# Kernel tuning notes

Measured on AMD Instinct MI355X. Metric: run time of the kernel, lower is better.

The kernel has to match this reference:

```python
import jax, jax.numpy as jnp
import numpy as np
import math

B, S, D, H, DFF = 4, 1024, 1024, 16, 4096
DK = D // H
EPS = 1e-5


def setup_inputs() -> dict:
    key = jax.random.key(0)
    ks = jax.random.split(key, 16)
    sc = 0.02
    inp = {
        "x": jax.random.normal(ks[0], (B, S, D), jnp.float32),
        "Wq": jax.random.normal(ks[1], (D, D), jnp.float32) * sc,
        "bq": jnp.zeros((D,), jnp.float32),
        "Wk": jax.random.normal(ks[2], (D, D), jnp.float32) * sc,
        "bk": jnp.zeros((D,), jnp.float32),
        "Wv": jax.random.normal(ks[3], (D, D), jnp.float32) * sc,
        "bv": jnp.zeros((D,), jnp.float32),
        "Wo": jax.random.normal(ks[4], (D, D), jnp.float32) * sc,
        "bo": jnp.zeros((D,), jnp.float32),
        "W1": jax.random.normal(ks[5], (D, DFF), jnp.float32) * sc,
        "b1": jnp.zeros((DFF,), jnp.float32),
        "W2": jax.random.normal(ks[6], (DFF, D), jnp.float32) * sc,
        "b2": jnp.zeros((D,), jnp.float32),
        "g1": jnp.ones((D,), jnp.float32),
        "be1": jnp.zeros((D,), jnp.float32),
        "g2": jnp.ones((D,), jnp.float32),
        "be2": jnp.zeros((D,), jnp.float32),
    }
    return inp


def _layernorm(x, g, b):
    mu = jnp.mean(x, axis=-1, keepdims=True)
    var = jnp.mean(jnp.square(x - mu), axis=-1, keepdims=True)
    return (x - mu) * jax.lax.rsqrt(var + EPS) * g + b


def reference(x, Wq, bq, Wk, bk, Wv, bv, Wo, bo, W1, b1, W2, b2, g1, be1, g2, be2):
    # multi-head self-attention (dropout = identity, eval mode)
    q = (x @ Wq + bq).reshape(B, S, H, DK).transpose(0, 2, 1, 3)  # [B,H,S,DK]
    k = (x @ Wk + bk).reshape(B, S, H, DK).transpose(0, 2, 1, 3)
    v = (x @ Wv + bv).reshape(B, S, H, DK).transpose(0, 2, 1, 3)
    scores = jnp.einsum("bhqd,bhkd->bhqk", q, k) / math.sqrt(DK)
    attn_weights = jax.nn.softmax(scores, axis=-1)
    ctx = jnp.einsum("bhqk,bhkd->bhqd", attn_weights, v)
    ctx = ctx.transpose(0, 2, 1, 3).reshape(B, S, D)
    attn_out = ctx @ Wo + bo
    x = _layernorm(x + attn_out, g1, be1)
    ff = jax.nn.relu(x @ W1 + b1) @ W2 + b2
    x = _layernorm(x + ff, g2, be2)
    return x, attn_weights
```

## Files before the change

### kernel.cpp

```cpp
#include <hip/hip_runtime.h>

typedef unsigned short u16;
typedef __attribute__((ext_vector_type(8))) short bf16x8;
typedef __attribute__((ext_vector_type(8))) unsigned short u16x8;
typedef __attribute__((ext_vector_type(4))) float f32x4;

__device__ __forceinline__ u16 f2b(float f) {
  unsigned u = __float_as_uint(f);
  u += 0x7fffu + ((u >> 16) & 1u);
  return (u16)(u >> 16);
}

__global__ __launch_bounds__(256) void cast_k(const float* __restrict__ s,
                                              u16* __restrict__ d, int n4) {
  int i = blockIdx.x * 256 + threadIdx.x;
  if (i >= n4) return;
  float4 v = *(const float4*)(s + (size_t)i * 4);
  ushort4 o = make_ushort4(f2b(v.x), f2b(v.y), f2b(v.z), f2b(v.w));
  *(ushort4*)(d + (size_t)i * 4) = o;
}

__global__ __launch_bounds__(256) void transpose_k(const float* __restrict__ src,
                                                   u16* __restrict__ dst,
                                                   int ldsrc, int lddst) {
  __shared__ float t[32][33];
  int c0 = blockIdx.x * 32, r0 = blockIdx.y * 32;
  int tx = threadIdx.x, ty = threadIdx.y;
#pragma unroll
  for (int i = 0; i < 4; ++i)
    t[ty + i * 8][tx] = src[(size_t)(r0 + ty + i * 8) * ldsrc + c0 + tx];
  __syncthreads();
#pragma unroll
  for (int i = 0; i < 4; ++i)
    dst[(size_t)(c0 + ty + i * 8) * lddst + r0 + tx] = f2b(t[tx][ty + i * 8]);
}

__global__ __launch_bounds__(256) void transpose_v_k(const u16* __restrict__ qkv,
                                                     u16* __restrict__ vt) {
  __shared__ u16 t[32][33];
  int z = blockIdx.z;
  int b = z >> 4, h = z & 15;
  int s0 = blockIdx.x * 32, d0 = blockIdx.y * 32;
  int tx = threadIdx.x, ty = threadIdx.y;
  const u16* src = qkv + (size_t)(b * 1024) * 3072 + 2048 + h * 64;
  u16* dst = vt + (size_t)z * 65536;
#pragma unroll
  for (int i = 0; i < 4; ++i)
    t[ty + i * 8][tx] = src[(size_t)(s0 + ty + i * 8) * 3072 + d0 + tx];
  __syncthreads();
#pragma unroll
  for (int i = 0; i < 4; ++i)
    dst[(size_t)(d0 + ty + i * 8) * 1024 + s0 + tx] = t[tx][ty + i * 8];
}

template <int BN, int AF32, int BIAS, int RELU, int SB16, int SF32>
__global__ __launch_bounds__(256) void gemm_k(
    const u16* __restrict__ Ab, const float* __restrict__ Af,
    long aHi, long aLo, int lda,
    const u16* __restrict__ Bt, long bHi, long bLo, int ldb,
    float* __restrict__ Cf, u16* __restrict__ Cb,
    long cHi, long cLo, int ldc,
    const float* __restrict__ bias, int K, int ZD) {
  constexpr int NT = BN / 32;
  __shared__ u16 As[128 * 40];
  __shared__ u16 Bs[BN * 40];

  const int tid = threadIdx.x;
  const int lane = tid & 63;
  const int wave = tid >> 6;
  const int waveM = wave >> 1, waveN = wave & 1;
  const int quad = lane >> 4, l16 = lane & 15;

  const int zb = blockIdx.z / ZD, zr = blockIdx.z % ZD;
  const long aOff = zb * aHi + zr * aLo;
  const long bOff = zb * bHi + zr * bLo;
  const long cOff = zb * cHi + zr * cLo;

  const int row0 = blockIdx.y * 128;
  const int col0 = blockIdx.x * BN;

  f32x4 acc[4][NT] = {};

  for (int k0 = 0; k0 < K; k0 += 32) {
#pragma unroll
    for (int it = 0; it < 2; ++it) {
      int e = (it * 256 + tid) * 8;
      int r = e >> 5, c = e & 31;
      if (AF32) {
        const float4* p = (const float4*)(Af + aOff + (long)(row0 + r) * lda + k0 + c);
        float4 v0 = p[0], v1 = p[1];
        u16x8 wv;
        wv[0] = f2b(v0.x); wv[1] = f2b(v0.y); wv[2] = f2b(v0.z); wv[3] = f2b(v0.w);
        wv[4] = f2b(v1.x); wv[5] = f2b(v1.y); wv[6] = f2b(v1.z); wv[7] = f2b(v1.w);
        *(u16x8*)&As[r * 40 + c] = wv;
      } else {
        uint4 v = *(const uint4*)(Ab + aOff + (long)(row0 + r) * lda + k0 + c);
        *(uint4*)&As[r * 40 + c] = v;
      }
    }
#pragma unroll
    for (int it = 0; it < BN / 64; ++it) {
      int e = (it * 256 + tid) * 8;
      int r = e >> 5, c = e & 31;
      uint4 v = *(const uint4*)(Bt + bOff + (long)(col0 + r) * ldb + k0 + c);
      *(uint4*)&Bs[r * 40 + c] = v;
    }
    __syncthreads();

    bf16x8 af[4], bfr[NT];
#pragma unroll
    for (int mi = 0; mi < 4; ++mi)
      af[mi] = *(const bf16x8*)&As[(waveM * 64 + mi * 16 + l16) * 40 + quad * 8];
#pragma unroll
    for (int ni = 0; ni < NT; ++ni)
      bfr[ni] = *(const bf16x8*)&Bs[(waveN * (BN / 2) + ni * 16 + l16) * 40 + quad * 8];
#pragma unroll
    for (int mi = 0; mi < 4; ++mi)
#pragma unroll
      for (int ni = 0; ni < NT; ++ni)
        acc[mi][ni] = __builtin_amdgcn_mfma_f32_16x16x32_bf16(af[mi], bfr[ni], acc[mi][ni], 0, 0, 0);
    __syncthreads();
  }

#pragma unroll
  for (int ni = 0; ni < NT; ++ni) {
    int col = col0 + waveN * (BN / 2) + ni * 16 + l16;
    float bv = BIAS ? bias[col] : 0.f;
#pragma unroll
    for (int mi = 0; mi < 4; ++mi) {
#pragma unroll
      for (int r = 0; r < 4; ++r) {
        int row = row0 + waveM * 64 + mi * 16 + quad * 4 + r;
        float v = acc[mi][ni][r] + bv;
        if (RELU) v = fmaxf(v, 0.f);
        long idx = cOff + (long)row * ldc + col;
        if (SF32) Cf[idx] = v;
        if (SB16) Cb[idx] = f2b(v);
      }
    }
  }
}

__global__ __launch_bounds__(256) void softmax_k(float* __restrict__ a) {
  long row = blockIdx.x;
  int tid = threadIdx.x;
  float* p = a + row * 1024 + tid * 4;
  float4 v = *(const float4*)p;
  float m = fmaxf(fmaxf(v.x, v.y), fmaxf(v.z, v.w));
#pragma unroll
  for (int d = 32; d > 0; d >>= 1) m = fmaxf(m, __shfl_xor(m, d));
  __shared__ float red[4];
  if ((tid & 63) == 0) red[tid >> 6] = m;
  __syncthreads();
  m = fmaxf(fmaxf(red[0], red[1]), fmaxf(red[2], red[3]));
  v.x = __expf((v.x - m) * 0.125f);
  v.y = __expf((v.y - m) * 0.125f);
  v.z = __expf((v.z - m) * 0.125f);
  v.w = __expf((v.w - m) * 0.125f);
  float s = v.x + v.y + v.z + v.w;
#pragma unroll
  for (int d = 32; d > 0; d >>= 1) s += __shfl_xor(s, d);
  __shared__ float red2[4];
  if ((tid & 63) == 0) red2[tid >> 6] = s;
  __syncthreads();
  s = red2[0] + red2[1] + red2[2] + red2[3];
  float r = 1.f / s;
  v.x *= r; v.y *= r; v.z *= r; v.w *= r;
  *(float4*)p = v;
}

template <int WB16>
__global__ __launch_bounds__(256) void add_ln_k(const float* __restrict__ xp,
                                                const float* __restrict__ yp,
                                                const float* __restrict__ g,
                                                const float* __restrict__ bta,
                                                float* __restrict__ of,
                                                u16* __restrict__ ob) {
  long row = blockIdx.x;
  int tid = threadIdx.x;
  const float4 xv = *(const float4*)(xp + row * 1024 + tid * 4);
  const float4 yv = *(const float4*)(yp + row * 1024 + tid * 4);
  float4 v = make_float4(xv.x + yv.x, xv.y + yv.y, xv.z + yv.z, xv.w + yv.w);
  float s1 = v.x + v.y + v.z + v.w;
  float s2 = v.x * v.x + v.y * v.y + v.z * v.z + v.w * v.w;
#pragma unroll
  for (int d = 32; d > 0; d >>= 1) {
    s1 += __shfl_xor(s1, d);
    s2 += __shfl_xor(s2, d);
  }
  __shared__ float r1[4], r2[4];
  if ((tid & 63) == 0) { r1[tid >> 6] = s1; r2[tid >> 6] = s2; }
  __syncthreads();
  s1 = r1[0] + r1[1] + r1[2] + r1[3];
  s2 = r2[0] + r2[1] + r2[2] + r2[3];
  float mu = s1 * (1.f / 1024.f);
  float var = s2 * (1.f / 1024.f) - mu * mu;
  float rs = rsqrtf(var + 1e-5f);
  float4 gv = *(const float4*)(g + tid * 4);
  float4 bv = *(const float4*)(bta + tid * 4);
  float4 o;
  o.x = (v.x - mu) * rs * gv.x + bv.x;
  o.y = (v.y - mu) * rs * gv.y + bv.y;
  o.z = (v.z - mu) * rs * gv.z + bv.z;
  o.w = (v.w - mu) * rs * gv.w + bv.w;
  *(float4*)(of + row * 1024 + tid * 4) = o;
  if (WB16) {
    ushort4 ov = make_ushort4(f2b(o.x), f2b(o.y), f2b(o.z), f2b(o.w));
    *(ushort4*)(ob + row * 1024 + tid * 4) = ov;
  }
}

extern "C" void kernel_launch(void* const* d_in, const int* in_sizes, int n_in,
                              void* d_out, int out_size, void* d_ws, size_t ws_size,
                              hipStream_t stream) {
  const float* x   = (const float*)d_in[0];
  const float* Wq  = (const float*)d_in[1];
  const float* bq  = (const float*)d_in[2];
  const float* Wk  = (const float*)d_in[3];
  const float* bk  = (const float*)d_in[4];
  const float* Wv  = (const float*)d_in[5];
  const float* bv  = (const float*)d_in[6];
  const float* Wo  = (const float*)d_in[7];
  const float* bo  = (const float*)d_in[8];
  const float* W1  = (const float*)d_in[9];
  const float* b1  = (const float*)d_in[10];
  const float* W2  = (const float*)d_in[11];
  const float* b2  = (const float*)d_in[12];
  const float* g1  = (const float*)d_in[13];
  const float* be1 = (const float*)d_in[14];
  const float* g2  = (const float*)d_in[15];
  const float* be2 = (const float*)d_in[16];

  float* out = (float*)d_out;
  float* attn = out + 4194304LL;

  char* w = (char*)d_ws;
  size_t off = 0;
  auto alloc = [&](size_t bytes) {
    void* p = w + off;
    off = (off + bytes + 255) & ~(size_t)255;
    return p;
  };
  u16* xb        = (u16*)alloc(8388608);
  u16* Wqkvt     = (u16*)alloc(6291456);
  u16* Wot       = (u16*)alloc(2097152);
  u16* W1t       = (u16*)alloc(8388608);
  u16* W2t       = (u16*)alloc(8388608);
  float* bqkv    = (float*)alloc(12288);
  u16* qkvb      = (u16*)alloc(25165824);
  u16* vtb       = (u16*)alloc(8388608);
  u16* ctxb      = (u16*)alloc(8388608);
  float* attn_o  = (float*)alloc(16777216);
  float* x1      = (float*)alloc(16777216);
  u16* x1b       = (u16*)alloc(8388608);
  u16* ff1b      = (u16*)alloc(33554432);
  float* ff2     = (float*)alloc(16777216);
  (void)ws_size; (void)in_sizes; (void)n_in; (void)out_size;

  dim3 tb(32, 8);
  cast_k<<<4096, 256, 0, stream>>>(x, xb, 1048576);
  transpose_k<<<dim3(32, 32), tb, 0, stream>>>(Wq, Wqkvt,           1024, 1024);
  transpose_k<<<dim3(32, 32), tb, 0, stream>>>(Wk, Wqkvt + 1048576, 1024, 1024);
  transpose_k<<<dim3(32, 32), tb, 0, stream>>>(Wv, Wqkvt + 2097152, 1024, 1024);
  transpose_k<<<dim3(32, 32), tb, 0, stream>>>(Wo, Wot, 1024, 1024);
  transpose_k<<<dim3(128, 32), tb, 0, stream>>>(W1, W1t, 4096, 1024);
  transpose_k<<<dim3(32, 128), tb, 0, stream>>>(W2, W2t, 1024, 4096);
  hipMemcpyAsync(bqkv,        bq, 4096, hipMemcpyDeviceToDevice, stream);
  hipMemcpyAsync(bqkv + 1024, bk, 4096, hipMemcpyDeviceToDevice, stream);
  hipMemcpyAsync(bqkv + 2048, bv, 4096, hipMemcpyDeviceToDevice, stream);

  gemm_k<128, 0, 1, 0, 1, 0><<<dim3(24, 32, 1), 256, 0, stream>>>(
      xb, nullptr, 0, 0, 1024, Wqkvt, 0, 0, 1024,
      nullptr, qkvb, 0, 0, 3072, bqkv, 1024, 1);

  transpose_v_k<<<dim3(32, 2, 64), tb, 0, stream>>>(qkvb, vtb);

  gemm_k<128, 0, 0, 0, 0, 1><<<dim3(8, 8, 64), 256, 0, stream>>>(
      qkvb, nullptr, 3145728, 64, 3072,
      qkvb + 1024, 3145728, 64, 3072,
      attn, nullptr, 16777216, 1048576, 1024, nullptr, 64, 16);

  softmax_k<<<65536, 256, 0, stream>>>(attn);

  gemm_k<64, 1, 0, 0, 1, 0><<<dim3(1, 8, 64), 256, 0, stream>>>(
      nullptr, attn, 16777216, 1048576, 1024,
      vtb, 1048576, 65536, 1024,
      nullptr, ctxb, 1048576, 64, 1024, nullptr, 1024, 16);

  gemm_k<128, 0, 1, 0, 0, 1><<<dim3(8, 32, 1), 256, 0, stream>>>(
      ctxb, nullptr, 0, 0, 1024, Wot, 0, 0, 1024,
      attn_o, nullptr, 0, 0, 1024, bo, 1024, 1);

  add_ln_k<1><<<4096, 256, 0, stream>>>(x, attn_o, g1, be1, x1, x1b);

  gemm_k<128, 0, 1, 1, 1, 0><<<dim3(32, 32, 1), 256, 0, stream>>>(
      x1b, nullptr, 0, 0, 1024, W1t, 0, 0, 1024,
      nullptr, ff1b, 0, 0, 4096, b1, 1024, 1);

  gemm_k<128, 0, 1, 0, 0, 1><<<dim3(8, 32, 1), 256, 0, stream>>>(
      ff1b, nullptr, 0, 0, 4096, W2t, 0, 0, 4096,
      ff2, nullptr, 0, 0, 1024, b2, 4096, 1);

  add_ln_k<0><<<4096, 256, 0, stream>>>(x1, ff2, g2, be2, out, nullptr);
}
```

Before: 822.7 us.

## Use direct global-to-LDS loads in GEMM and restructure softmax via fused exp

The GEMM kernel now stages tiles with global_load_lds 16-byte loads into unpadded LDS, and its K-step goes from 32 to 64 with two MFMA sub-steps per tile. Softmax is split up: the QK^T GEMM applies exp(score/8) in its epilogue and writes bf16, a light norm kernel computes row sums and writes the normalized fp32 weights plus the inverse sums, and the PV GEMM reads the bf16 exponentials and scales each row by the inverse sum. This drops the fp32 read-modify-write pass over the 256MB attention matrix and the fp32-to-bf16 conversion in the PV A-loads. In exchange, the max subtraction is gone, which risks overflow for large scores, and the unpadded LDS layout may cause bank conflicts.

```diff
diff --git a/kernel.cpp b/kernel.cpp
--- a/kernel.cpp
+++ b/kernel.cpp
@@ -2,13 +2,20 @@
 
 typedef unsigned short u16;
 typedef __attribute__((ext_vector_type(8))) short bf16x8;
-typedef __attribute__((ext_vector_type(8))) unsigned short u16x8;
 typedef __attribute__((ext_vector_type(4))) float f32x4;
 
 __device__ __forceinline__ u16 f2b(float f) {
   unsigned u = __float_as_uint(f);
   u += 0x7fffu + ((u >> 16) & 1u);
   return (u16)(u >> 16);
+}
+__device__ __forceinline__ float b2f(u16 v) {
+  return __uint_as_float((unsigned)v << 16);
+}
+
+__device__ __forceinline__ void gload16(const u16* g, u16* l) {
+  __builtin_amdgcn_global_load_lds((__attribute__((address_space(1))) void*)(g),
+                                   (__attribute__((address_space(3))) void*)(l), 16, 0, 0);
 }
 
 __global__ __launch_bounds__(256) void cast_k(const float* __restrict__ s,
@@ -53,17 +60,18 @@
     dst[(size_t)(d0 + ty + i * 8) * 1024 + s0 + tx] = t[tx][ty + i * 8];
 }
 
-template <int BN, int AF32, int BIAS, int RELU, int SB16, int SF32>
+template <int BN, int BIAS, int RELU, int EXPE, int RSCALE, int SB16, int SF32>
 __global__ __launch_bounds__(256) void gemm_k(
-    const u16* __restrict__ Ab, const float* __restrict__ Af,
-    long aHi, long aLo, int lda,
+    const u16* __restrict__ Ab, long aHi, long aLo, int lda,
     const u16* __restrict__ Bt, long bHi, long bLo, int ldb,
     float* __restrict__ Cf, u16* __restrict__ Cb,
     long cHi, long cLo, int ldc,
-    const float* __restrict__ bias, int K, int ZD) {
+    const float* __restrict__ bias, const float* __restrict__ rs,
+    int K, int ZD) {
   constexpr int NT = BN / 32;
-  __shared__ u16 As[128 * 40];
-  __shared__ u16 Bs[BN * 40];
+  constexpr int CB = (BN * 64 * 2) / 1024;
+  __shared__ __align__(128) u16 As[128 * 64];
+  __shared__ __align__(128) u16 Bs[BN * 64];
 
   const int tid = threadIdx.x;
   const int lane = tid & 63;
@@ -79,46 +87,44 @@
   const int row0 = blockIdx.y * 128;
   const int col0 = blockIdx.x * BN;
 
+  const int lr = lane >> 3;
+  const int lc = (lane & 7) * 8;
+
   f32x4 acc[4][NT] = {};
 
-  for (int k0 = 0; k0 < K; k0 += 32) {
-#pragma unroll
-    for (int it = 0; it < 2; ++it) {
-      int e = (it * 256 + tid) * 8;
-      int r = e >> 5, c = e & 31;
-      if (AF32) {
-        const float4* p = (const float4*)(Af + aOff + (long)(row0 + r) * lda + k0 + c);
-        float4 v0 = p[0], v1 = p[1];
-        u16x8 wv;
-        wv[0] = f2b(v0.x); wv[1] = f2b(v0.y); wv[2] = f2b(v0.z); wv[3] = f2b(v0.w);
-        wv[4] = f2b(v1.x); wv[5] = f2b(v1.y); wv[6] = f2b(v1.z); wv[7] = f2b(v1.w);
-        *(u16x8*)&As[r * 40 + c] = wv;
-      } else {
-        uint4 v = *(const uint4*)(Ab + aOff + (long)(row0 + r) * lda + k0 + c);
-        *(uint4*)&As[r * 40 + c] = v;
-      }
+  for (int k0 = 0; k0 < K; k0 += 64) {
+    const u16* Ag = Ab + aOff + (long)row0 * lda + k0;
+    const u16* Bg = Bt + bOff + (long)col0 * ldb + k0;
+#pragma unroll
+    for (int c = 0; c < 4; ++c) {
+      int ch = c * 4 + wave;
+      gload16(Ag + (long)(ch * 8 + lr) * lda + lc, &As[ch * 512]);
     }
 #pragma unroll
-    for (int it = 0; it < BN / 64; ++it) {
-      int e = (it * 256 + tid) * 8;
-      int r = e >> 5, c = e & 31;
-      uint4 v = *(const uint4*)(Bt + bOff + (long)(col0 + r) * ldb + k0 + c);
-      *(uint4*)&Bs[r * 40 + c] = v;
+    for (int c = 0; c < CB / 4; ++c) {
+      int ch = c * 4 + wave;
+      gload16(Bg + (long)(ch * 8 + lr) * ldb + lc, &Bs[ch * 512]);
     }
     __syncthreads();
 
-    bf16x8 af[4], bfr[NT];
+    bf16x8 af[4][2], bfr[NT][2];
 #pragma unroll
     for (int mi = 0; mi < 4; ++mi)
-      af[mi] = *(const bf16x8*)&As[(waveM * 64 + mi * 16 + l16) * 40 + quad * 8];
+#pragma unroll
+      for (int ks = 0; ks < 2; ++ks)
+        af[mi][ks] = *(const bf16x8*)&As[(waveM * 64 + mi * 16 + l16) * 64 + ks * 32 + quad * 8];
 #pragma unroll
     for (int ni = 0; ni < NT; ++ni)
-      bfr[ni] = *(const bf16x8*)&Bs[(waveN * (BN / 2) + ni * 16 + l16) * 40 + quad * 8];
-#pragma unroll
-    for (int mi = 0; mi < 4; ++mi)
-#pragma unroll
-      for (int ni = 0; ni < NT; ++ni)
-        acc[mi][ni] = __builtin_amdgcn_mfma_f32_16x16x32_bf16(af[mi], bfr[ni], acc[mi][ni], 0, 0, 0);
+#pragma unroll
+      for (int ks = 0; ks < 2; ++ks)
+        bfr[ni][ks] = *(const bf16x8*)&Bs[(waveN * (BN / 2) + ni * 16 + l16) * 64 + ks * 32 + quad * 8];
+#pragma unroll
+    for (int ks = 0; ks < 2; ++ks)
+#pragma unroll
+      for (int mi = 0; mi < 4; ++mi)
+#pragma unroll
+        for (int ni = 0; ni < NT; ++ni)
+          acc[mi][ni] = __builtin_amdgcn_mfma_f32_16x16x32_bf16(af[mi][ks], bfr[ni][ks], acc[mi][ni], 0, 0, 0);
     __syncthreads();
   }
 
@@ -133,6 +139,8 @@
         int row = row0 + waveM * 64 + mi * 16 + quad * 4 + r;
         float v = acc[mi][ni][r] + bv;
         if (RELU) v = fmaxf(v, 0.f);
+        if (EXPE) v = __expf(v * 0.125f);
+        if (RSCALE) v *= rs[(long)blockIdx.z * 1024 + row];
         long idx = cOff + (long)row * ldc + col;
         if (SF32) Cf[idx] = v;
         if (SB16) Cb[idx] = f2b(v);
@@ -141,32 +149,25 @@
   }
 }
 
-__global__ __launch_bounds__(256) void softmax_k(float* __restrict__ a) {
+__global__ __launch_bounds__(256) void norm_k(const u16* __restrict__ e,
+                                              float* __restrict__ w,
+                                              float* __restrict__ inv) {
   long row = blockIdx.x;
   int tid = threadIdx.x;
-  float* p = a + row * 1024 + tid * 4;
-  float4 v = *(const float4*)p;
-  float m = fmaxf(fmaxf(v.x, v.y), fmaxf(v.z, v.w));
-#pragma unroll
-  for (int d = 32; d > 0; d >>= 1) m = fmaxf(m, __shfl_xor(m, d));
+  ushort4 ev = *(const ushort4*)(e + row * 1024 + tid * 4);
+  float4 v;
+  v.x = b2f(ev.x); v.y = b2f(ev.y); v.z = b2f(ev.z); v.w = b2f(ev.w);
+  float s = v.x + v.y + v.z + v.w;
+#pragma unroll
+  for (int d = 32; d > 0; d >>= 1) s += __shfl_xor(s, d);
   __shared__ float red[4];
-  if ((tid & 63) == 0) red[tid >> 6] = m;
+  if ((tid & 63) == 0) red[tid >> 6] = s;
   __syncthreads();
-  m = fmaxf(fmaxf(red[0], red[1]), fmaxf(red[2], red[3]));
-  v.x = __expf((v.x - m) * 0.125f);
-  v.y = __expf((v.y - m) * 0.125f);
-  v.z = __expf((v.z - m) * 0.125f);
-  v.w = __expf((v.w - m) * 0.125f);
-  float s = v.x + v.y + v.z + v.w;
-#pragma unroll
-  for (int d = 32; d > 0; d >>= 1) s += __shfl_xor(s, d);
-  __shared__ float red2[4];
-  if ((tid & 63) == 0) red2[tid >> 6] = s;
-  __syncthreads();
-  s = red2[0] + red2[1] + red2[2] + red2[3];
+  s = red[0] + red[1] + red[2] + red[3];
   float r = 1.f / s;
-  v.x *= r; v.y *= r; v.z *= r; v.w *= r;
-  *(float4*)p = v;
+  float4 o = make_float4(v.x * r, v.y * r, v.z * r, v.w * r);
+  *(float4*)(w + row * 1024 + tid * 4) = o;
+  if (tid == 0) inv[row] = r;
 }
 
 template <int WB16>
@@ -249,6 +250,8 @@
   float* bqkv    = (float*)alloc(12288);
   u16* qkvb      = (u16*)alloc(25165824);
   u16* vtb       = (u16*)alloc(8388608);
+  u16* expb      = (u16*)alloc(134217728);
+  float* inv     = (float*)alloc(262144);
   u16* ctxb      = (u16*)alloc(8388608);
   float* attn_o  = (float*)alloc(16777216);
   float* x1      = (float*)alloc(16777216);
@@ -269,37 +272,37 @@
   hipMemcpyAsync(bqkv + 1024, bk, 4096, hipMemcpyDeviceToDevice, stream);
   hipMemcpyAsync(bqkv + 2048, bv, 4096, hipMemcpyDeviceToDevice, stream);
 
-  gemm_k<128, 0, 1, 0, 1, 0><<<dim3(24, 32, 1), 256, 0, stream>>>(
-      xb, nullptr, 0, 0, 1024, Wqkvt, 0, 0, 1024,
-      nullptr, qkvb, 0, 0, 3072, bqkv, 1024, 1);
+  gemm_k<128, 1, 0, 0, 0, 1, 0><<<dim3(24, 32, 1), 256, 0, stream>>>(
+      xb, 0, 0, 1024, Wqkvt, 0, 0, 1024,
+      nullptr, qkvb, 0, 0, 3072, bqkv, nullptr, 1024, 1);
 
   transpose_v_k<<<dim3(32, 2, 64), tb, 0, stream>>>(qkvb, vtb);
 
-  gemm_k<128, 0, 0, 0, 0, 1><<<dim3(8, 8, 64), 256, 0, stream>>>(
-      qkvb, nullptr, 3145728, 64, 3072,
-      qkvb + 1024, 3145728, 64, 3072,
-      attn, nullptr, 16777216, 1048576, 1024, nullptr, 64, 16);
-
-  softmax_k<<<65536, 256, 0, stream>>>(attn);
-
-  gemm_k<64, 1, 0, 0, 1, 0><<<dim3(1, 8, 64), 256, 0, stream>>>(
-      nullptr, attn, 16777216, 1048576, 1024,
-      vtb, 1048576, 65536, 1024,
-      nullptr, ctxb, 1048576, 64, 1024, nullptr, 1024, 16);
-
-  gemm_k<128, 0, 1, 0, 0, 1><<<dim3(8, 32, 1), 256, 0, stream>>>(
-      ctxb, nullptr, 0, 0, 1024, Wot, 0, 0, 1024,
-      attn_o, nullptr, 0, 0, 1024, bo, 1024, 1);
+  gemm_k<128, 0, 0, 1, 0, 1, 0><<<dim3(8, 8, 64), 256, 0, stream>>>(
+      qkvb, 3145728L, 64, 3072,
+      qkvb + 1024, 3145728L, 64, 3072,
+      nullptr, expb, 16777216L, 1048576L, 1024, nullptr, nullptr, 64, 16);
+
+  norm_k<<<65536, 256, 0, stream>>>(expb, attn, inv);
+
+  gemm_k<64, 0, 0, 0, 1, 1, 0><<<dim3(1, 8, 64), 256, 0, stream>>>(
+      expb, 16777216L, 1048576L, 1024,
+      vtb, 1048576L, 65536L, 1024,
+      nullptr, ctxb, 1048576L, 64, 1024, nullptr, inv, 1024, 16);
+
+  gemm_k<128, 1, 0, 0, 0, 0, 1><<<dim3(8, 32, 1), 256, 0, stream>>>(
+      ctxb, 0, 0, 1024, Wot, 0, 0, 1024,
+      attn_o, nullptr, 0, 0, 1024, bo, nullptr, 1024, 1);
 
   add_ln_k<1><<<4096, 256, 0, stream>>>(x, attn_o, g1, be1, x1, x1b);
 
-  gemm_k<128, 0, 1, 1, 1, 0><<<dim3(32, 32, 1), 256, 0, stream>>>(
-      x1b, nullptr, 0, 0, 1024, W1t, 0, 0, 1024,
-      nullptr, ff1b, 0, 0, 4096, b1, 1024, 1);
-
-  gemm_k<128, 0, 1, 0, 0, 1><<<dim3(8, 32, 1), 256, 0, stream>>>(
-      ff1b, nullptr, 0, 0, 4096, W2t, 0, 0, 4096,
-      ff2, nullptr, 0, 0, 1024, b2, 4096, 1);
+  gemm_k<128, 1, 1, 0, 0, 1, 0><<<dim3(32, 32, 1), 256, 0, stream>>>(
+      x1b, 0, 0, 1024, W1t, 0, 0, 1024,
+      nullptr, ff1b, 0, 0, 4096, b1, nullptr, 1024, 1);
+
+  gemm_k<128, 1, 0, 0, 0, 0, 1><<<dim3(8, 32, 1), 256, 0, stream>>>(
+      ff1b, 0, 0, 4096, W2t, 0, 0, 4096,
+      ff2, nullptr, 0, 0, 1024, b2, nullptr, 4096, 1);
 
   add_ln_k<0><<<4096, 256, 0, stream>>>(x1, ff2, g2, be2, out, nullptr);
 }
```

Result: faster. 753.9 us (-8.4%).
